# Optimization experiments

Measured on AMD Instinct MI355X. Metric: run time of the kernel, lower is better.

Reference implementation:

```python
import jax, jax.numpy as jnp
import numpy as np

N_NODES = 30000
N_EDGES = 480000
NEG_SLOPE = 0.2  # PyG GATConv default negative_slope


def setup_inputs() -> dict:
    key = jax.random.key(0)
    ks = jax.random.split(key, 10)

    def glorot(k, shape, fan):
        return jax.random.normal(k, shape, jnp.float32) * (1.0 / np.sqrt(fan))

    x = jax.random.normal(ks[0], (N_NODES, 1024), jnp.float32)
    edge_index = jax.random.randint(ks[1], (2, N_EDGES), 0, N_NODES)
    # layer 1: in=1024 -> heads=8, C=64, concat -> 512
    W1 = glorot(ks[2], (1024, 512), 1024)
    a1_src = glorot(ks[3], (8, 64), 64)
    a1_dst = glorot(ks[4], (8, 64), 64)
    b1 = jnp.zeros((512,), jnp.float32)
    # layer 2: in=512 -> heads=1, C=256, no concat
    W2 = glorot(ks[5], (512, 256), 512)
    a2_src = glorot(ks[6], (1, 256), 256)
    a2_dst = glorot(ks[7], (1, 256), 256)
    b2 = jnp.zeros((256,), jnp.float32)
    return {"x": x, "edge_index": edge_index, "W1": W1, "a1_src": a1_src,
            "a1_dst": a1_dst, "b1": b1, "W2": W2, "a2_src": a2_src,
            "a2_dst": a2_dst, "b2": b2}


def gat_conv(x, src, dst, W, a_src, a_dst, bias, heads, channels, concat):
    """PyG-style GATConv (self-loops already included in src/dst)."""
    n = x.shape[0]
    h = (x @ W).reshape(n, heads, channels)          # [N, H, C]
    al_s = jnp.einsum('nhc,hc->nh', h, a_src)        # per-node src logits
    al_d = jnp.einsum('nhc,hc->nh', h, a_dst)        # per-node dst logits
    e = jax.nn.leaky_relu(al_s[src] + al_d[dst], NEG_SLOPE)   # [E, H]
    # segment softmax over edges grouped by destination node
    m = jax.ops.segment_max(e, dst, num_segments=n)
    p = jnp.exp(e - m[dst])
    s = jax.ops.segment_sum(p, dst, num_segments=n)
    alpha = p / s[dst]                               # [E, H]
    out = jax.ops.segment_sum(alpha[:, :, None] * h[src], dst, num_segments=n)
    out = out.reshape(n, heads * channels) if concat else out.mean(axis=1)
    return out + bias


def reference(x, edge_index, W1, a1_src, a1_dst, b1, W2, a2_src, a2_dst, b2):
    n = x.shape[0]
    loops = jnp.arange(n, dtype=edge_index.dtype)
    src = jnp.concatenate([edge_index[0], loops])    # add self-loops (PyG default)
    dst = jnp.concatenate([edge_index[1], loops])
    # eval mode: dropout is identity
    h = jax.nn.elu(gat_conv(x, src, dst, W1, a1_src, a1_dst, b1, 8, 64, True))
    out = gat_conv(h, src, dst, W2, a2_src, a2_dst, b2, 1, 256, False)
    return out
```

## Files before the change

kernel.cpp:

```cpp
#include <hip/hip_runtime.h>
#include <hip/hip_bf16.h>

typedef unsigned int uint;
typedef unsigned short ushort;
typedef __attribute__((ext_vector_type(8))) short short8;
typedef __attribute__((ext_vector_type(4))) short short4v;
typedef __attribute__((ext_vector_type(4))) float f32x4;

#define LEAKY 0.2f

__device__ __forceinline__ ushort f2bf(float f) {
  __hip_bfloat16 h = __float2bfloat16(f);
  return __builtin_bit_cast(ushort, h);
}
__device__ __forceinline__ float bf2f(ushort u) {
  uint v = ((uint)u) << 16;
  return __builtin_bit_cast(float, v);
}
__device__ __forceinline__ void gload_lds16(const void* g, void* l) {
  __builtin_amdgcn_global_load_lds(
      (const __attribute__((address_space(1))) void*)g,
      (__attribute__((address_space(3))) void*)l, 16, 0, 0);
}

__global__ void convw_all(const float* __restrict__ W1, ushort* __restrict__ W1t,
                          const float* __restrict__ W2, ushort* __restrict__ W2t) {
  int idx = blockIdx.x * 256 + threadIdx.x;
  const int n1 = 512 * 1024;
  if (idx < n1) {
    int nrow = idx >> 10, k = idx & 1023;
    W1t[idx] = f2bf(W1[(size_t)k * 512 + nrow]);
  } else {
    idx -= n1;
    if (idx < 256 * 512) {
      int nrow = idx >> 9, k = idx & 511;
      W2t[idx] = f2bf(W2[(size_t)k * 256 + nrow]);
    }
  }
}

__global__ void zero2(int* a, int* b, int n) {
  int i = blockIdx.x * 256 + threadIdx.x;
  if (i < n) { a[i] = 0; b[i] = 0; }
}

__global__ void hist(const int* __restrict__ dst, int E, int n, int* cnt) {
  int e = blockIdx.x * 256 + threadIdx.x;
  if (e >= E + n) return;
  int d = (e < E) ? dst[e] : (e - E);
  atomicAdd(&cnt[d], 1);
}

__global__ __launch_bounds__(1024) void scan_fast(const int* __restrict__ cnt,
                                                  int* __restrict__ rp, int n) {
  __shared__ int wsum[16];
  __shared__ int woff[16];
  const int t = threadIdx.x;
  const int per = (n + 1023) / 1024;
  const int base = t * per;
  int local[32];
  int s = 0;
#pragma unroll
  for (int i = 0; i < 32; i++) {
    if (i >= per) break;
    int idx = base + i;
    int v = (idx < n) ? cnt[idx] : 0;
    local[i] = s;
    s += v;
  }
  const int lane = t & 63, wave = t >> 6;
  int incl = s;
#pragma unroll
  for (int off = 1; off < 64; off <<= 1) {
    int v = __shfl_up(incl, off);
    if (lane >= off) incl += v;
  }
  if (lane == 63) wsum[wave] = incl;
  __syncthreads();
  if (wave == 0 && lane < 16) {
    int v = wsum[lane];
    int wi = v;
#pragma unroll
    for (int off = 1; off < 16; off <<= 1) {
      int u = __shfl_up(wi, off);
      if (lane >= off) wi += u;
    }
    woff[lane] = wi - v;
  }
  __syncthreads();
  const int gexcl = woff[wave] + (incl - s);
#pragma unroll
  for (int i = 0; i < 32; i++) {
    if (i >= per) break;
    int idx = base + i;
    if (idx < n) rp[idx] = gexcl + local[i];
  }
  if (t == 1023) rp[n] = woff[15] + incl;
}

__global__ void scatter(const int* __restrict__ src, const int* __restrict__ dst,
                        int E, int n, const int* __restrict__ rp,
                        int* fill, int* __restrict__ csr) {
  int e = blockIdx.x * 256 + threadIdx.x;
  if (e >= E + n) return;
  int s, d;
  if (e < E) { s = src[e]; d = dst[e]; } else { s = d = e - E; }
  int pos = rp[d] + atomicAdd(&fill[d], 1);
  csr[pos] = s;
}

template <int ABYTES, int HEADS>
__global__ __launch_bounds__(512) void gemm_fl(
    const void* __restrict__ Av, const ushort* __restrict__ Bt,
    ushort* __restrict__ C, float* __restrict__ al_s, float* __restrict__ al_d,
    const float* __restrict__ as_vec, const float* __restrict__ ad_vec,
    int M, int K, int N) {
  constexpr int BM = 128, BN = 256, BK = 32;
  constexpr int SPRA = (BK * ABYTES) / 16;
  constexpr int A_ITER = (BM * SPRA) / 512;
  __shared__ __align__(16) char As[BM * BK * ABYTES];
  __shared__ __align__(16) char Bs[BN * BK * 2];
  const int tid = threadIdx.x;
  const int wave = tid >> 6, lane = tid & 63;
  const int g = lane >> 4, r16 = lane & 15;
  const int nby = N / BN;
  const int bx = (int)blockIdx.x / nby;
  const int by = (int)blockIdx.x - bx * nby;
  const int bm = bx * BM, bn = by * BN;
  const int wm = (wave >> 2) * 64, wn = (wave & 3) * 64;

  f32x4 acc[4][4] = {};
  const char* A = (const char*)Av;

  for (int k0 = 0; k0 < K; k0 += BK) {
#pragma unroll
    for (int i = 0; i < A_ITER; i++) {
      int slot = i * 512 + tid;
      int row = slot / SPRA;
      int cp = slot - row * SPRA;
      int key = (ABYTES == 4) ? (row & 7) : ((row >> 1) & 3);
      int cl = cp ^ key;
      int arow = bm + row;
      arow = arow < M ? arow : M - 1;
      const char* gp = A + ((size_t)arow * K + k0) * ABYTES + cl * 16;
      char* lp = As + (i * 512 + wave * 64) * 16;
      gload_lds16(gp, lp);
    }
#pragma unroll
    for (int i = 0; i < 2; i++) {
      int slot = i * 512 + tid;
      int row = slot >> 2;
      int cp = slot & 3;
      int cl = cp ^ ((row >> 1) & 3);
      const char* gp = (const char*)(Bt + (size_t)(bn + row) * K + k0 + cl * 8);
      char* lp = Bs + (i * 512 + wave * 64) * 16;
      gload_lds16(gp, lp);
    }
    asm volatile("s_waitcnt vmcnt(0)" ::: "memory");
    __syncthreads();

    short8 af[4], bfr[4];
#pragma unroll
    for (int mi = 0; mi < 4; mi++) {
      int row = wm + mi * 16 + r16;
      if constexpr (ABYTES == 4) {
        int key = row & 7;
        f32x4 lo = *(const f32x4*)(As + (row * 8 + ((2 * g) ^ key)) * 16);
        f32x4 hi = *(const f32x4*)(As + (row * 8 + ((2 * g + 1) ^ key)) * 16);
        short8 s;
#pragma unroll
        for (int qq = 0; qq < 4; qq++) {
          s[qq] = (short)f2bf(lo[qq]);
          s[qq + 4] = (short)f2bf(hi[qq]);
        }
        af[mi] = s;
      } else {
        int key = (row >> 1) & 3;
        af[mi] = *(const short8*)(As + (row * 4 + (g ^ key)) * 16);
      }
    }
#pragma unroll
    for (int ni = 0; ni < 4; ni++) {
      int row = wn + ni * 16 + r16;
      int key = (row >> 1) & 3;
      bfr[ni] = *(const short8*)(Bs + (row * 4 + (g ^ key)) * 16);
    }
#pragma unroll
    for (int mi = 0; mi < 4; mi++)
#pragma unroll
      for (int ni = 0; ni < 4; ni++)
        acc[mi][ni] = __builtin_amdgcn_mfma_f32_16x16x32_bf16(
            af[mi], bfr[ni], acc[mi][ni], 0, 0, 0);
    __syncthreads();
  }

#pragma unroll
  for (int mi = 0; mi < 4; mi++) {
#pragma unroll
    for (int j = 0; j < 4; j++) {
      int row = bm + wm + mi * 16 + g * 4 + j;
      if (row < M) {
#pragma unroll
        for (int ni = 0; ni < 4; ni++) {
          int col = bn + wn + ni * 16 + r16;
          C[(size_t)row * N + col] = f2bf(acc[mi][ni][j]);
        }
      }
    }
  }

  if constexpr (HEADS == 8) {
    const int head = (bn + wn) >> 6;
    float asr[4], adr[4];
#pragma unroll
    for (int ni = 0; ni < 4; ni++) {
      asr[ni] = as_vec[head * 64 + ni * 16 + r16];
      adr[ni] = ad_vec[head * 64 + ni * 16 + r16];
    }
#pragma unroll
    for (int mi = 0; mi < 4; mi++) {
#pragma unroll
      for (int j = 0; j < 4; j++) {
        float ps = 0.f, pd = 0.f;
#pragma unroll
        for (int ni = 0; ni < 4; ni++) {
          ps += acc[mi][ni][j] * asr[ni];
          pd += acc[mi][ni][j] * adr[ni];
        }
#pragma unroll
        for (int off = 1; off < 16; off <<= 1) {
          ps += __shfl_xor(ps, off);
          pd += __shfl_xor(pd, off);
        }
        if (r16 == 0) {
          int row = bm + wm + mi * 16 + g * 4 + j;
          if (row < M) {
            al_s[row * 8 + head] = ps;
            al_d[row * 8 + head] = pd;
          }
        }
      }
    }
  } else {
    float* sred = (float*)As;
    float* dred = sred + 512;
    float asr[4], adr[4];
#pragma unroll
    for (int ni = 0; ni < 4; ni++) {
      asr[ni] = as_vec[wn + ni * 16 + r16];
      adr[ni] = ad_vec[wn + ni * 16 + r16];
    }
    __syncthreads();
#pragma unroll
    for (int mi = 0; mi < 4; mi++) {
#pragma unroll
      for (int j = 0; j < 4; j++) {
        float ps = 0.f, pd = 0.f;
#pragma unroll
        for (int ni = 0; ni < 4; ni++) {
          ps += acc[mi][ni][j] * asr[ni];
          pd += acc[mi][ni][j] * adr[ni];
        }
#pragma unroll
        for (int off = 1; off < 16; off <<= 1) {
          ps += __shfl_xor(ps, off);
          pd += __shfl_xor(pd, off);
        }
        if (r16 == 0) {
          int rloc = mi * 16 + g * 4 + j;
          sred[wave * 64 + rloc] = ps;
          dred[wave * 64 + rloc] = pd;
        }
      }
    }
    __syncthreads();
    if (tid < 128) {
      int base = (tid >= 64) ? 4 : 0;
      int rl = tid & 63;
      float s = sred[(base + 0) * 64 + rl] + sred[(base + 1) * 64 + rl] +
                sred[(base + 2) * 64 + rl] + sred[(base + 3) * 64 + rl];
      float d = dred[(base + 0) * 64 + rl] + dred[(base + 1) * 64 + rl] +
                dred[(base + 2) * 64 + rl] + dred[(base + 3) * 64 + rl];
      int row = bm + tid;
      if (row < M) {
        al_s[row] = s;
        al_d[row] = d;
      }
    }
  }
}

__global__ void agg1(const int* __restrict__ rp, const int* __restrict__ csr,
                     const ushort* __restrict__ h1, const float* __restrict__ al_s,
                     const float* __restrict__ al_d, const float* __restrict__ b1,
                     ushort* __restrict__ h2in, int n) {
  int node = blockIdx.x * 4 + (threadIdx.x >> 6);
  if (node >= n) return;
  int lane = threadIdx.x & 63;
  int head = lane >> 3, c0 = lane * 8;
  float ad = al_d[node * 8 + head];
  int beg = rp[node], end = rp[node + 1];
  float sum = 0.f;
  float acc[8] = {};
  int j = beg;
  for (; j + 4 <= end; j += 4) {
    int s0 = csr[j], s1 = csr[j + 1], s2 = csr[j + 2], s3 = csr[j + 3];
    float e0 = al_s[s0 * 8 + head] + ad;
    float e1 = al_s[s1 * 8 + head] + ad;
    float e2 = al_s[s2 * 8 + head] + ad;
    float e3 = al_s[s3 * 8 + head] + ad;
    short8 v0 = *(const short8*)&h1[(size_t)s0 * 512 + c0];
    short8 v1 = *(const short8*)&h1[(size_t)s1 * 512 + c0];
    short8 v2 = *(const short8*)&h1[(size_t)s2 * 512 + c0];
    short8 v3 = *(const short8*)&h1[(size_t)s3 * 512 + c0];
    e0 = e0 > 0.f ? e0 : LEAKY * e0;
    e1 = e1 > 0.f ? e1 : LEAKY * e1;
    e2 = e2 > 0.f ? e2 : LEAKY * e2;
    e3 = e3 > 0.f ? e3 : LEAKY * e3;
    float p0 = __expf(e0), p1 = __expf(e1), p2 = __expf(e2), p3 = __expf(e3);
    sum += (p0 + p1) + (p2 + p3);
#pragma unroll
    for (int qq = 0; qq < 8; qq++)
      acc[qq] += p0 * bf2f((ushort)v0[qq]) + p1 * bf2f((ushort)v1[qq]) +
                 p2 * bf2f((ushort)v2[qq]) + p3 * bf2f((ushort)v3[qq]);
  }
  for (; j < end; j++) {
    int s = csr[j];
    float e = al_s[s * 8 + head] + ad;
    e = e > 0.f ? e : LEAKY * e;
    float p = __expf(e);
    sum += p;
    short8 hv = *(const short8*)&h1[(size_t)s * 512 + c0];
#pragma unroll
    for (int qq = 0; qq < 8; qq++) acc[qq] += p * bf2f((ushort)hv[qq]);
  }
  float inv = 1.0f / sum;
  short8 o;
#pragma unroll
  for (int qq = 0; qq < 8; qq++) {
    float rr = acc[qq] * inv + b1[c0 + qq];
    rr = rr > 0.f ? rr : (__expf(rr) - 1.0f);
    o[qq] = (short)f2bf(rr);
  }
  *(short8*)&h2in[(size_t)node * 512 + c0] = o;
}

__global__ void agg2(const int* __restrict__ rp, const int* __restrict__ csr,
                     const ushort* __restrict__ h2, const float* __restrict__ al_s,
                     const float* __restrict__ al_d, const float* __restrict__ b2,
                     float* __restrict__ out, int n) {
  int node = blockIdx.x * 4 + (threadIdx.x >> 6);
  if (node >= n) return;
  int lane = threadIdx.x & 63;
  int c0 = lane * 4;
  float ad = al_d[node];
  int beg = rp[node], end = rp[node + 1];
  float sum = 0.f;
  float a0 = 0.f, a1 = 0.f, a2 = 0.f, a3 = 0.f;
  int j = beg;
  for (; j + 4 <= end; j += 4) {
    int s0 = csr[j], s1 = csr[j + 1], s2 = csr[j + 2], s3 = csr[j + 3];
    float e0 = al_s[s0] + ad;
    float e1 = al_s[s1] + ad;
    float e2 = al_s[s2] + ad;
    float e3 = al_s[s3] + ad;
    short4v v0 = *(const short4v*)&h2[(size_t)s0 * 256 + c0];
    short4v v1 = *(const short4v*)&h2[(size_t)s1 * 256 + c0];
    short4v v2 = *(const short4v*)&h2[(size_t)s2 * 256 + c0];
    short4v v3 = *(const short4v*)&h2[(size_t)s3 * 256 + c0];
    e0 = e0 > 0.f ? e0 : LEAKY * e0;
    e1 = e1 > 0.f ? e1 : LEAKY * e1;
    e2 = e2 > 0.f ? e2 : LEAKY * e2;
    e3 = e3 > 0.f ? e3 : LEAKY * e3;
    float p0 = __expf(e0), p1 = __expf(e1), p2 = __expf(e2), p3 = __expf(e3);
    sum += (p0 + p1) + (p2 + p3);
    a0 += p0 * bf2f((ushort)v0[0]) + p1 * bf2f((ushort)v1[0]) +
          p2 * bf2f((ushort)v2[0]) + p3 * bf2f((ushort)v3[0]);
    a1 += p0 * bf2f((ushort)v0[1]) + p1 * bf2f((ushort)v1[1]) +
          p2 * bf2f((ushort)v2[1]) + p3 * bf2f((ushort)v3[1]);
    a2 += p0 * bf2f((ushort)v0[2]) + p1 * bf2f((ushort)v1[2]) +
          p2 * bf2f((ushort)v2[2]) + p3 * bf2f((ushort)v3[2]);
    a3 += p0 * bf2f((ushort)v0[3]) + p1 * bf2f((ushort)v1[3]) +
          p2 * bf2f((ushort)v2[3]) + p3 * bf2f((ushort)v3[3]);
  }
  for (; j < end; j++) {
    int s = csr[j];
    float e = al_s[s] + ad;
    e = e > 0.f ? e : LEAKY * e;
    float p = __expf(e);
    sum += p;
    short4v hv = *(const short4v*)&h2[(size_t)s * 256 + c0];
    a0 += p * bf2f((ushort)hv[0]);
    a1 += p * bf2f((ushort)hv[1]);
    a2 += p * bf2f((ushort)hv[2]);
    a3 += p * bf2f((ushort)hv[3]);
  }
  float inv = 1.0f / sum;
  f32x4 o;
  o[0] = a0 * inv + b2[c0 + 0];
  o[1] = a1 * inv + b2[c0 + 1];
  o[2] = a2 * inv + b2[c0 + 2];
  o[3] = a3 * inv + b2[c0 + 3];
  *(f32x4*)&out[(size_t)node * 256 + c0] = o;
}

extern "C" void kernel_launch(void* const* d_in, const int* in_sizes, int n_in,
                              void* d_out, int out_size, void* d_ws, size_t ws_size,
                              hipStream_t stream) {
  const float* x = (const float*)d_in[0];
  const int* ei = (const int*)d_in[1];
  const float* W1 = (const float*)d_in[2];
  const float* a1s = (const float*)d_in[3];
  const float* a1d = (const float*)d_in[4];
  const float* b1 = (const float*)d_in[5];
  const float* W2 = (const float*)d_in[6];
  const float* a2s = (const float*)d_in[7];
  const float* a2d = (const float*)d_in[8];
  const float* b2 = (const float*)d_in[9];
  float* out = (float*)d_out;

  const int n = in_sizes[0] / 1024;
  const int E = in_sizes[1] / 2;
  const int K1 = 1024, C1 = 512, C2 = 256;

  char* ws = (char*)d_ws;
  ushort* h1 = (ushort*)(ws + 0);
  ushort* h2in = (ushort*)(ws + 31000000);
  ushort* h2 = (ushort*)(ws + 62000000);
  float* al_s = (float*)(ws + 78000000);
  float* al_d = (float*)(ws + 79000000);
  float* al2s = (float*)(ws + 80000000);
  float* al2d = (float*)(ws + 80200000);
  ushort* W1t = (ushort*)(ws + 80400000);
  ushort* W2t = (ushort*)(ws + 81600000);
  int* cnt = (int*)(ws + 82000000);
  int* rp = (int*)(ws + 82200000);
  int* fill = (int*)(ws + 82400000);
  int* csr = (int*)(ws + 82600000);

  const int* esrc = ei;
  const int* edst = ei + E;
  const int ET = E + n;

  convw_all<<<(C1 * K1 + C2 * C1 + 255) / 256, 256, 0, stream>>>(W1, W1t, W2, W2t);
  zero2<<<(n + 255) / 256, 256, 0, stream>>>(cnt, fill, n);
  hist<<<(ET + 255) / 256, 256, 0, stream>>>(edst, E, n, cnt);
  scan_fast<<<1, 1024, 0, stream>>>(cnt, rp, n);
  scatter<<<(ET + 255) / 256, 256, 0, stream>>>(esrc, edst, E, n, rp, fill, csr);

  const int gx1 = ((n + 127) / 128) * (C1 / 256);
  gemm_fl<4, 8><<<gx1, 512, 0, stream>>>(x, W1t, h1, al_s, al_d, a1s, a1d, n, K1, C1);
  agg1<<<(n + 3) / 4, 256, 0, stream>>>(rp, csr, h1, al_s, al_d, b1, h2in, n);

  const int gx2 = ((n + 127) / 128) * (C2 / 256);
  gemm_fl<2, 1><<<gx2, 512, 0, stream>>>(h2in, W2t, h2, al2s, al2d, a2s, a2d, n, C1, C2);
  agg2<<<(n + 3) / 4, 256, 0, stream>>>(rp, csr, h2, al2s, al2d, b2, out, n);
}
```

Measured before the change: 272.7 us.

## Double GEMM row tile to 256 with 1024-thread blocks and widen aggregation unroll

The GEMM block grows to 256x256 with 16 waves, so each B tile is loaded once per 256 rows instead of 128, and the epilogue reduction is adjusted for the extra waves. The aggregation kernels now batch 8 neighbor index, logit and feature loads before accumulating, which puts more gathers in flight. The costs are fewer GEMM blocks (lower occupancy and less tail balance on a 30000-row problem), more LDS per block, and higher register pressure in the gather loops.

After: 296.5 us. 1.09x slower.

```diff
diff --git a/kernel.cpp b/kernel.cpp
--- a/kernel.cpp
+++ b/kernel.cpp
@@ -110,14 +110,14 @@
 }
 
 template <int ABYTES, int HEADS>
-__global__ __launch_bounds__(512) void gemm_fl(
+__global__ __launch_bounds__(1024) void gemm_fl(
     const void* __restrict__ Av, const ushort* __restrict__ Bt,
     ushort* __restrict__ C, float* __restrict__ al_s, float* __restrict__ al_d,
     const float* __restrict__ as_vec, const float* __restrict__ ad_vec,
     int M, int K, int N) {
-  constexpr int BM = 128, BN = 256, BK = 32;
+  constexpr int BM = 256, BN = 256, BK = 32;
   constexpr int SPRA = (BK * ABYTES) / 16;
-  constexpr int A_ITER = (BM * SPRA) / 512;
+  constexpr int A_ITER = (BM * SPRA) / 1024;
   __shared__ __align__(16) char As[BM * BK * ABYTES];
   __shared__ __align__(16) char Bs[BN * BK * 2];
   const int tid = threadIdx.x;
@@ -135,7 +135,7 @@
   for (int k0 = 0; k0 < K; k0 += BK) {
 #pragma unroll
     for (int i = 0; i < A_ITER; i++) {
-      int slot = i * 512 + tid;
+      int slot = i * 1024 + tid;
       int row = slot / SPRA;
       int cp = slot - row * SPRA;
       int key = (ABYTES == 4) ? (row & 7) : ((row >> 1) & 3);
@@ -143,17 +143,16 @@
       int arow = bm + row;
       arow = arow < M ? arow : M - 1;
       const char* gp = A + ((size_t)arow * K + k0) * ABYTES + cl * 16;
-      char* lp = As + (i * 512 + wave * 64) * 16;
+      char* lp = As + (i * 1024 + wave * 64) * 16;
       gload_lds16(gp, lp);
     }
-#pragma unroll
-    for (int i = 0; i < 2; i++) {
-      int slot = i * 512 + tid;
+    {
+      int slot = tid;
       int row = slot >> 2;
       int cp = slot & 3;
       int cl = cp ^ ((row >> 1) & 3);
       const char* gp = (const char*)(Bt + (size_t)(bn + row) * K + k0 + cl * 8);
-      char* lp = Bs + (i * 512 + wave * 64) * 16;
+      char* lp = Bs + (size_t)(wave * 64) * 16;
       gload_lds16(gp, lp);
     }
     asm volatile("s_waitcnt vmcnt(0)" ::: "memory");
@@ -243,7 +242,7 @@
     }
   } else {
     float* sred = (float*)As;
-    float* dred = sred + 512;
+    float* dred = sred + 16 * 64;
     float asr[4], adr[4];
 #pragma unroll
     for (int ni = 0; ni < 4; ni++) {
@@ -274,13 +273,14 @@
       }
     }
     __syncthreads();
-    if (tid < 128) {
-      int base = (tid >= 64) ? 4 : 0;
+    if (tid < 256) {
+      int wg = tid >> 6;
       int rl = tid & 63;
-      float s = sred[(base + 0) * 64 + rl] + sred[(base + 1) * 64 + rl] +
-                sred[(base + 2) * 64 + rl] + sred[(base + 3) * 64 + rl];
-      float d = dred[(base + 0) * 64 + rl] + dred[(base + 1) * 64 + rl] +
-                dred[(base + 2) * 64 + rl] + dred[(base + 3) * 64 + rl];
+      int w0 = wg * 4;
+      float s = sred[(w0 + 0) * 64 + rl] + sred[(w0 + 1) * 64 + rl] +
+                sred[(w0 + 2) * 64 + rl] + sred[(w0 + 3) * 64 + rl];
+      float d = dred[(w0 + 0) * 64 + rl] + dred[(w0 + 1) * 64 + rl] +
+                dred[(w0 + 2) * 64 + rl] + dred[(w0 + 3) * 64 + rl];
       int row = bm + tid;
       if (row < M) {
         al_s[row] = s;
@@ -303,26 +303,25 @@
   float sum = 0.f;
   float acc[8] = {};
   int j = beg;
-  for (; j + 4 <= end; j += 4) {
-    int s0 = csr[j], s1 = csr[j + 1], s2 = csr[j + 2], s3 = csr[j + 3];
-    float e0 = al_s[s0 * 8 + head] + ad;
-    float e1 = al_s[s1 * 8 + head] + ad;
-    float e2 = al_s[s2 * 8 + head] + ad;
-    float e3 = al_s[s3 * 8 + head] + ad;
-    short8 v0 = *(const short8*)&h1[(size_t)s0 * 512 + c0];
-    short8 v1 = *(const short8*)&h1[(size_t)s1 * 512 + c0];
-    short8 v2 = *(const short8*)&h1[(size_t)s2 * 512 + c0];
-    short8 v3 = *(const short8*)&h1[(size_t)s3 * 512 + c0];
-    e0 = e0 > 0.f ? e0 : LEAKY * e0;
-    e1 = e1 > 0.f ? e1 : LEAKY * e1;
-    e2 = e2 > 0.f ? e2 : LEAKY * e2;
-    e3 = e3 > 0.f ? e3 : LEAKY * e3;
-    float p0 = __expf(e0), p1 = __expf(e1), p2 = __expf(e2), p3 = __expf(e3);
-    sum += (p0 + p1) + (p2 + p3);
-#pragma unroll
-    for (int qq = 0; qq < 8; qq++)
-      acc[qq] += p0 * bf2f((ushort)v0[qq]) + p1 * bf2f((ushort)v1[qq]) +
-                 p2 * bf2f((ushort)v2[qq]) + p3 * bf2f((ushort)v3[qq]);
+  for (; j + 8 <= end; j += 8) {
+    int sx[8];
+    float e[8];
+    short8 v[8];
+#pragma unroll
+    for (int u = 0; u < 8; u++) sx[u] = csr[j + u];
+#pragma unroll
+    for (int u = 0; u < 8; u++) e[u] = al_s[sx[u] * 8 + head] + ad;
+#pragma unroll
+    for (int u = 0; u < 8; u++) v[u] = *(const short8*)&h1[(size_t)sx[u] * 512 + c0];
+#pragma unroll
+    for (int u = 0; u < 8; u++) {
+      float eu = e[u];
+      eu = eu > 0.f ? eu : LEAKY * eu;
+      float p = __expf(eu);
+      sum += p;
+#pragma unroll
+      for (int qq = 0; qq < 8; qq++) acc[qq] += p * bf2f((ushort)v[u][qq]);
+    }
   }
   for (; j < end; j++) {
     int s = csr[j];
@@ -358,30 +357,27 @@
   float sum = 0.f;
   float a0 = 0.f, a1 = 0.f, a2 = 0.f, a3 = 0.f;
   int j = beg;
-  for (; j + 4 <= end; j += 4) {
-    int s0 = csr[j], s1 = csr[j + 1], s2 = csr[j + 2], s3 = csr[j + 3];
-    float e0 = al_s[s0] + ad;
-    float e1 = al_s[s1] + ad;
-    float e2 = al_s[s2] + ad;
-    float e3 = al_s[s3] + ad;
-    short4v v0 = *(const short4v*)&h2[(size_t)s0 * 256 + c0];
-    short4v v1 = *(const short4v*)&h2[(size_t)s1 * 256 + c0];
-    short4v v2 = *(const short4v*)&h2[(size_t)s2 * 256 + c0];
-    short4v v3 = *(const short4v*)&h2[(size_t)s3 * 256 + c0];
-    e0 = e0 > 0.f ? e0 : LEAKY * e0;
-    e1 = e1 > 0.f ? e1 : LEAKY * e1;
-    e2 = e2 > 0.f ? e2 : LEAKY * e2;
-    e3 = e3 > 0.f ? e3 : LEAKY * e3;
-    float p0 = __expf(e0), p1 = __expf(e1), p2 = __expf(e2), p3 = __expf(e3);
-    sum += (p0 + p1) + (p2 + p3);
-    a0 += p0 * bf2f((ushort)v0[0]) + p1 * bf2f((ushort)v1[0]) +
-          p2 * bf2f((ushort)v2[0]) + p3 * bf2f((ushort)v3[0]);
-    a1 += p0 * bf2f((ushort)v0[1]) + p1 * bf2f((ushort)v1[1]) +
-          p2 * bf2f((ushort)v2[1]) + p3 * bf2f((ushort)v3[1]);
-    a2 += p0 * bf2f((ushort)v0[2]) + p1 * bf2f((ushort)v1[2]) +
-          p2 * bf2f((ushort)v2[2]) + p3 * bf2f((ushort)v3[2]);
-    a3 += p0 * bf2f((ushort)v0[3]) + p1 * bf2f((ushort)v1[3]) +
-          p2 * bf2f((ushort)v2[3]) + p3 * bf2f((ushort)v3[3]);
+  for (; j + 8 <= end; j += 8) {
+    int sx[8];
+    float e[8];
+    short4v v[8];
+#pragma unroll
+    for (int u = 0; u < 8; u++) sx[u] = csr[j + u];
+#pragma unroll
+    for (int u = 0; u < 8; u++) e[u] = al_s[sx[u]] + ad;
+#pragma unroll
+    for (int u = 0; u < 8; u++) v[u] = *(const short4v*)&h2[(size_t)sx[u] * 256 + c0];
+#pragma unroll
+    for (int u = 0; u < 8; u++) {
+      float eu = e[u];
+      eu = eu > 0.f ? eu : LEAKY * eu;
+      float p = __expf(eu);
+      sum += p;
+      a0 += p * bf2f((ushort)v[u][0]);
+      a1 += p * bf2f((ushort)v[u][1]);
+      a2 += p * bf2f((ushort)v[u][2]);
+      a3 += p * bf2f((ushort)v[u][3]);
+    }
   }
   for (; j < end; j++) {
     int s = csr[j];
@@ -448,11 +444,11 @@
   scan_fast<<<1, 1024, 0, stream>>>(cnt, rp, n);
   scatter<<<(ET + 255) / 256, 256, 0, stream>>>(esrc, edst, E, n, rp, fill, csr);
 
-  const int gx1 = ((n + 127) / 128) * (C1 / 256);
-  gemm_fl<4, 8><<<gx1, 512, 0, stream>>>(x, W1t, h1, al_s, al_d, a1s, a1d, n, K1, C1);
+  const int gx1 = ((n + 255) / 256) * (C1 / 256);
+  gemm_fl<4, 8><<<gx1, 1024, 0, stream>>>(x, W1t, h1, al_s, al_d, a1s, a1d, n, K1, C1);
   agg1<<<(n + 3) / 4, 256, 0, stream>>>(rp, csr, h1, al_s, al_d, b1, h2in, n);
 
-  const int gx2 = ((n + 127) / 128) * (C2 / 256);
-  gemm_fl<2, 1><<<gx2, 512, 0, stream>>>(h2in, W2t, h2, al2s, al2d, a2s, a2d, n, C1, C2);
+  const int gx2 = ((n + 255) / 256) * (C2 / 256);
+  gemm_fl<2, 1><<<gx2, 1024, 0, stream>>>(h2in, W2t, h2, al2s, al2d, a2s, a2d, n, C1, C2);
   agg2<<<(n + 3) / 4, 256, 0, stream>>>(rp, csr, h2, al2s, al2d, b2, out, n);
 }
```
